# Performance work log

Measured on AMD Instinct MI355X. Metric: run time of the kernel, lower is better.

Reference implementation:

```python
import jax, jax.numpy as jnp
from jax import lax
import numpy as np

CH = 512      # ch_in = c_in = c_out
P = 8         # p: channels per group
NG = CH // P  # depthwise groups
PG = CH // P  # pointwise groups
EPS = 1e-5
DN = ('NCHW', 'OIHW', 'NCHW')


def leaky(x):
    return jnp.where(x >= 0, x, 0.01 * x)  # LeakyReLU default slope


def setup_inputs() -> dict:
    key = jax.random.key(0)
    ks = jax.random.split(key, 8)
    N, H, W = 16, 64, 64
    return {
        'style_encoding': jax.random.normal(ks[0], (N, 512, 4, 4), jnp.float32),
        'content_in': jax.random.normal(ks[1], (N, CH, H, W), jnp.float32),
        'dw_w': jax.random.normal(ks[2], (P, 512, 2, 2), jnp.float32) * 0.05,
        'dw_b': jax.random.normal(ks[3], (P,), jnp.float32) * 0.05,
        'pk_w': jax.random.normal(ks[4], (P, 512), jnp.float32) * 0.05,
        'pk_b': jax.random.normal(ks[5], (P,), jnp.float32) * 0.05,
        'pb_w': jax.random.normal(ks[6], (CH, 512), jnp.float32) * 0.05,
        'pb_b': jax.random.normal(ks[7], (CH,), jnp.float32) * 0.05,
    }


def reference(style_encoding, content_in, dw_w, dw_b, pk_w, pk_b, pb_w, pb_b):
    N, _, H, W = content_in.shape
    # --- KernelPredictor ---
    # depthwise kernels: 2x2 valid conv on 4x4 style map -> [N, P, 3, 3]
    d = lax.conv_general_dilated(style_encoding, dw_w, (1, 1), 'VALID',
                                 dimension_numbers=DN)
    d = leaky(d + dw_b[None, :, None, None])  # [N, P, 3, 3]
    # expand: same [P,3,3] filter for every output channel -> [N, CH, P, 3, 3]
    depthwise = jnp.broadcast_to(d[:, None], (N, CH, P, 3, 3))
    # avg-pool 4 on 4x4 style map == global mean -> [N, 512]
    s_d = jnp.mean(style_encoding, axis=(2, 3))
    pk = jnp.einsum('nc,oc->no', s_d, pk_w) + pk_b       # [N, P]  (1x1 conv)
    bias = jnp.einsum('nc,oc->no', s_d, pb_w) + pb_b     # [N, CH] (1x1 conv)

    # --- per-sample grouped convs, batched by folding batch into groups ---
    padded = jnp.pad(content_in, ((0, 0), (0, 0), (1, 1), (1, 1)), mode='reflect')
    xr = padded.reshape(1, N * CH, H + 2, W + 2)
    wr = depthwise.reshape(N * CH, P, 3, 3)
    depth = lax.conv_general_dilated(xr, wr, (1, 1), 'VALID',
                                     feature_group_count=N * NG,
                                     dimension_numbers=DN)
    depth = depth.reshape(N, CH, H, W)

    # pointwise 1x1 grouped conv: weight [N, CH, P, 1, 1], identical over out
    # channels within a sample (expand); groups = PG, CH//PG == P out ch/group
    depth_g = depth.reshape(N, PG, P, H, W)
    pw_g = jnp.broadcast_to(pk[:, None, None, :], (N, PG, P, P))  # [n,g,o,j]
    out = jnp.einsum('ngjhw,ngoj->ngohw', depth_g, pw_g).reshape(N, CH, H, W)
    predicted = leaky(out + bias[:, :, None, None])

    # --- instance-norm of content (AdaIN calc_mean_std, unbiased var) ---
    mean = jnp.mean(content_in, axis=(2, 3), keepdims=True)
    std = jnp.sqrt(jnp.var(content_in, axis=(2, 3), keepdims=True, ddof=1) + EPS)
    normalized = (content_in - mean) / std
    return normalized * predicted
```

## Files before the change

kernel.cpp:

```cpp
#include <hip/hip_runtime.h>
#include <math.h>

#define CH 512
#define P 8
#define PLANE 4096
#define EPS 1e-5f

typedef float f4 __attribute__((ext_vector_type(4)));

__device__ __forceinline__ float leaky(float x) { return x >= 0.f ? x : 0.01f * x; }

__device__ __forceinline__ float wave_sum(float v) {
    #pragma unroll
    for (int off = 32; off; off >>= 1) v += __shfl_xor(v, off, 64);
    return v;
}

__global__ __launch_bounds__(256) void style_kernel(
    const float* __restrict__ style,
    const float* __restrict__ dw_w,
    const float* __restrict__ dw_b,
    const float* __restrict__ pk_w,
    const float* __restrict__ pk_b,
    float* __restrict__ sd_out,
    float* __restrict__ S_out,
    float* __restrict__ d_pred)
{
    const int blk = blockIdx.x;
    const int t = threadIdx.x;
    const int wave = t >> 6, lane = t & 63;

    __shared__ float s_sd[512];
    __shared__ float red[4];

    if (blk < 16) {
        const int n = blk;
        const float* sb = style + (size_t)n * 8192;
        #pragma unroll
        for (int qd = 0; qd < 2; ++qd) {
            int c = t + 256 * qd;
            const float4* sp = (const float4*)sb + c * 4;
            float4 a = sp[0], b = sp[1], d = sp[2], e = sp[3];
            float s = a.x + a.y + a.z + a.w + b.x + b.y + b.z + b.w
                    + d.x + d.y + d.z + d.w + e.x + e.y + e.z + e.w;
            s *= (1.f / 16.f);
            s_sd[c] = s;
            sd_out[n * 512 + c] = s;
        }
        __syncthreads();
        float part = 0.f;
        #pragma unroll
        for (int o = 0; o < 8; ++o)
            part += pk_w[o * 512 + t] * s_sd[t]
                  + pk_w[o * 512 + t + 256] * s_sd[t + 256];
        part = wave_sum(part);
        if (lane == 0) red[wave] = part;
        __syncthreads();
        if (t == 0) {
            float S = red[0] + red[1] + red[2] + red[3];
            #pragma unroll
            for (int o = 0; o < 8; ++o) S += pk_b[o];
            S_out[n] = S;
        }
    } else {
        const int W = (blk - 16) * 4 + wave;
        const int n = W / 72, r = W % 72;
        const int j = r / 9, pos = r % 9, y = pos / 3, x = pos % 3;
        const float* sb = style + (size_t)n * 8192;
        const float4* wp = (const float4*)dw_w;
        float acc = 0.f;
        #pragma unroll
        for (int i = 0; i < 8; ++i) {
            int c = lane + 64 * i;
            float4 w = wp[j * 512 + c];
            const float* s = sb + c * 16 + y * 4 + x;
            acc += s[0] * w.x + s[1] * w.y + s[4] * w.z + s[5] * w.w;
        }
        acc = wave_sum(acc);
        if (lane == 0) d_pred[n * 72 + r] = leaky(acc + dw_b[j]);
    }
}

__global__ __launch_bounds__(256) void bias_stats_kernel(
    const float* __restrict__ content,
    const float* __restrict__ sd,
    const float* __restrict__ pb_w,
    const float* __restrict__ pb_b,
    float* __restrict__ bias_out,
    float* __restrict__ mean_out,
    float* __restrict__ rstd_out)
{
    const int blk = blockIdx.x;
    const int t = threadIdx.x;
    const int wave = t >> 6, lane = t & 63;

    __shared__ float ls[4], lq[4];

    if (blk < 128) {
        const int c = blk * 4 + wave;
        float w[8];
        #pragma unroll
        for (int i = 0; i < 8; ++i) w[i] = pb_w[(size_t)c * 512 + lane + 64 * i];
        float acc[16];
        #pragma unroll
        for (int nn = 0; nn < 16; ++nn) acc[nn] = 0.f;
        #pragma unroll
        for (int i = 0; i < 8; ++i) {
            #pragma unroll
            for (int nn = 0; nn < 16; ++nn)
                acc[nn] += w[i] * sd[nn * 512 + lane + 64 * i];
        }
        #pragma unroll
        for (int nn = 0; nn < 16; ++nn) acc[nn] = wave_sum(acc[nn]);
        if (lane == 0) {
            float bb = pb_b[c];
            #pragma unroll
            for (int nn = 0; nn < 16; ++nn) bias_out[nn * 512 + c] = acc[nn] + bb;
        }
    } else {
        const int nc = blk - 128;
        const float4* base = (const float4*)(content + (size_t)nc * PLANE);
        float s = 0.f, sq = 0.f;
        #pragma unroll
        for (int k = 0; k < 4; ++k) {
            float4 v = base[k * 256 + t];
            s  += v.x + v.y + v.z + v.w;
            sq += v.x * v.x + v.y * v.y + v.z * v.z + v.w * v.w;
        }
        #pragma unroll
        for (int off = 32; off > 0; off >>= 1) {
            s  += __shfl_down(s, off, 64);
            sq += __shfl_down(sq, off, 64);
        }
        if (lane == 0) { ls[wave] = s; lq[wave] = sq; }
        __syncthreads();
        if (t == 0) {
            float S = ls[0] + ls[1] + ls[2] + ls[3];
            float Q = lq[0] + lq[1] + lq[2] + lq[3];
            float m = S * (1.f / 4096.f);
            float var = (Q - 4096.f * m * m) * (1.f / 4095.f);
            mean_out[nc] = m;
            rstd_out[nc] = rsqrtf(var + EPS);
        }
    }
}

__global__ __launch_bounds__(256, 4) void main_kernel(
    const float* __restrict__ content,
    const float* __restrict__ d_pred,
    const float* __restrict__ S_in,
    const float* __restrict__ bias_in,
    const float* __restrict__ mean_in,
    const float* __restrict__ rstd_in,
    float* __restrict__ out)
{
    const int b    = blockIdx.x;
    const int tile = b & 3;
    const int g    = (b >> 2) & 63;
    const int n    = b >> 8;
    const int t  = threadIdx.x;
    const int tx = t & 15, ty = t >> 4;
    const int h  = tile * 16 + ty;
    const int x0 = tx * 4;

    __shared__ float s_d[72];
    __shared__ float s_S;
    __shared__ float s_bias[8], s_mean[8], s_rstd[8];
    if (t < 72) s_d[t] = d_pred[n * 72 + t];
    if (t == 80) s_S = S_in[n];
    if (t >= 88 && t < 96) {
        int o = t - 88;
        int c = n * 512 + g * 8 + o;
        s_bias[o] = bias_in[c];
        s_mean[o] = mean_in[c];
        s_rstd[o] = rstd_in[c];
    }
    __syncthreads();

    const float* cbase = content + (size_t)(n * 512 + g * 8) * PLANE;
    const int ry0 = (h == 0)  ? 1  : h - 1;
    const int ry2 = (h == 63) ? 62 : h + 1;
    const int o0 = ry0 * 64 + x0;
    const int o1 = h   * 64 + x0;
    const int o2 = ry2 * 64 + x0;

    float D0 = 0.f, D1 = 0.f, D2 = 0.f, D3 = 0.f;
    f4 xc[8];

    #pragma unroll 2
    for (int j = 0; j < 8; ++j) {
        const float* cj = cbase + j * PLANE;
        f4 va = *(const f4*)(cj + o0);
        f4 vb = *(const f4*)(cj + o1);
        f4 vc = *(const f4*)(cj + o2);
        xc[j] = vb;
        const float* wj = s_d + j * 9;
        {
            float lv = __shfl_up(va.w, 1, 64);
            float rv = __shfl_down(va.x, 1, 64);
            float xm = (tx == 0)  ? va.y : lv;
            float xp = (tx == 15) ? va.z : rv;
            D0 += wj[0] * xm   + wj[1] * va.x + wj[2] * va.y;
            D1 += wj[0] * va.x + wj[1] * va.y + wj[2] * va.z;
            D2 += wj[0] * va.y + wj[1] * va.z + wj[2] * va.w;
            D3 += wj[0] * va.z + wj[1] * va.w + wj[2] * xp;
        }
        {
            float lv = __shfl_up(vb.w, 1, 64);
            float rv = __shfl_down(vb.x, 1, 64);
            float xm = (tx == 0)  ? vb.y : lv;
            float xp = (tx == 15) ? vb.z : rv;
            D0 += wj[3] * xm   + wj[4] * vb.x + wj[5] * vb.y;
            D1 += wj[3] * vb.x + wj[4] * vb.y + wj[5] * vb.z;
            D2 += wj[3] * vb.y + wj[4] * vb.z + wj[5] * vb.w;
            D3 += wj[3] * vb.z + wj[4] * vb.w + wj[5] * xp;
        }
        {
            float lv = __shfl_up(vc.w, 1, 64);
            float rv = __shfl_down(vc.x, 1, 64);
            float xm = (tx == 0)  ? vc.y : lv;
            float xp = (tx == 15) ? vc.z : rv;
            D0 += wj[6] * xm   + wj[7] * vc.x + wj[8] * vc.y;
            D1 += wj[6] * vc.x + wj[7] * vc.y + wj[8] * vc.z;
            D2 += wj[6] * vc.y + wj[7] * vc.z + wj[8] * vc.w;
            D3 += wj[6] * vc.z + wj[7] * vc.w + wj[8] * xp;
        }
    }

    const float S = s_S;
    const float P0 = D0 * S, P1 = D1 * S, P2 = D2 * S, P3 = D3 * S;
    float* obase = out + (size_t)(n * 512 + g * 8) * PLANE + h * 64 + x0;
    #pragma unroll
    for (int o = 0; o < 8; ++o) {
        float bb = s_bias[o], m = s_mean[o], rs = s_rstd[o];
        f4 res;
        res.x = (xc[o].x - m) * rs * leaky(P0 + bb);
        res.y = (xc[o].y - m) * rs * leaky(P1 + bb);
        res.z = (xc[o].z - m) * rs * leaky(P2 + bb);
        res.w = (xc[o].w - m) * rs * leaky(P3 + bb);
        __builtin_nontemporal_store(res, (f4*)(obase + o * PLANE));
    }
}

extern "C" void kernel_launch(void* const* d_in, const int* in_sizes, int n_in,
                              void* d_out, int out_size, void* d_ws, size_t ws_size,
                              hipStream_t stream) {
    const float* style   = (const float*)d_in[0];
    const float* content = (const float*)d_in[1];
    const float* dw_w    = (const float*)d_in[2];
    const float* dw_b    = (const float*)d_in[3];
    const float* pk_w    = (const float*)d_in[4];
    const float* pk_b    = (const float*)d_in[5];
    const float* pb_w    = (const float*)d_in[6];
    const float* pb_b    = (const float*)d_in[7];
    float* out = (float*)d_out;
    float* ws  = (float*)d_ws;

    const int N = 16;
    float* sd_ws   = ws;
    float* d_pred  = sd_ws + N * 512;
    float* S_ws    = d_pred + N * 72;
    float* bias_ws = S_ws + N;
    float* mean_ws = bias_ws + N * 512;
    float* rstd_ws = mean_ws + N * 512;

    style_kernel<<<16 + 288, 256, 0, stream>>>(style, dw_w, dw_b, pk_w, pk_b,
                                               sd_ws, S_ws, d_pred);
    bias_stats_kernel<<<128 + N * 512, 256, 0, stream>>>(
        content, sd_ws, pb_w, pb_b, bias_ws, mean_ws, rstd_ws);
    main_kernel<<<N * 64 * 4, 256, 0, stream>>>(content, d_pred, S_ws, bias_ws,
                                                mean_ws, rstd_ws, out);
}
```

Baseline: 265.9 us.

## Merge style and stats kernels; compute bias per block inside main kernel

Folds the content instance-norm statistics into the style prep kernel, which removes one launch and one serialization point. The pointwise-bias GEMV no longer runs as a separate pass: each main-kernel block now computes its own 8 bias values from pb_w and the style means before its barrier. This removes a kernel boundary and the bias workspace round trip. The cost is redundant bias computation, since the four tile blocks of each group and sample each repeat the 8x512 dot products, and that adds latency at block start.

Measured after the change: 266.0 us. About the same (+0.0%).

```diff
diff --git a/kernel.cpp b/kernel.cpp
--- a/kernel.cpp
+++ b/kernel.cpp
@@ -16,15 +16,18 @@
     return v;
 }
 
-__global__ __launch_bounds__(256) void style_kernel(
+__global__ __launch_bounds__(256) void prep_kernel(
     const float* __restrict__ style,
+    const float* __restrict__ content,
     const float* __restrict__ dw_w,
     const float* __restrict__ dw_b,
     const float* __restrict__ pk_w,
     const float* __restrict__ pk_b,
     float* __restrict__ sd_out,
     float* __restrict__ S_out,
-    float* __restrict__ d_pred)
+    float* __restrict__ d_pred,
+    float* __restrict__ mean_out,
+    float* __restrict__ rstd_out)
 {
     const int blk = blockIdx.x;
     const int t = threadIdx.x;
@@ -32,6 +35,7 @@
 
     __shared__ float s_sd[512];
     __shared__ float red[4];
+    __shared__ float ls[4], lq[4];
 
     if (blk < 16) {
         const int n = blk;
@@ -62,7 +66,7 @@
             for (int o = 0; o < 8; ++o) S += pk_b[o];
             S_out[n] = S;
         }
-    } else {
+    } else if (blk < 304) {
         const int W = (blk - 16) * 4 + wave;
         const int n = W / 72, r = W % 72;
         const int j = r / 9, pos = r % 9, y = pos / 3, x = pos % 3;
@@ -78,47 +82,8 @@
         }
         acc = wave_sum(acc);
         if (lane == 0) d_pred[n * 72 + r] = leaky(acc + dw_b[j]);
-    }
-}
-
-__global__ __launch_bounds__(256) void bias_stats_kernel(
-    const float* __restrict__ content,
-    const float* __restrict__ sd,
-    const float* __restrict__ pb_w,
-    const float* __restrict__ pb_b,
-    float* __restrict__ bias_out,
-    float* __restrict__ mean_out,
-    float* __restrict__ rstd_out)
-{
-    const int blk = blockIdx.x;
-    const int t = threadIdx.x;
-    const int wave = t >> 6, lane = t & 63;
-
-    __shared__ float ls[4], lq[4];
-
-    if (blk < 128) {
-        const int c = blk * 4 + wave;
-        float w[8];
-        #pragma unroll
-        for (int i = 0; i < 8; ++i) w[i] = pb_w[(size_t)c * 512 + lane + 64 * i];
-        float acc[16];
-        #pragma unroll
-        for (int nn = 0; nn < 16; ++nn) acc[nn] = 0.f;
-        #pragma unroll
-        for (int i = 0; i < 8; ++i) {
-            #pragma unroll
-            for (int nn = 0; nn < 16; ++nn)
-                acc[nn] += w[i] * sd[nn * 512 + lane + 64 * i];
-        }
-        #pragma unroll
-        for (int nn = 0; nn < 16; ++nn) acc[nn] = wave_sum(acc[nn]);
-        if (lane == 0) {
-            float bb = pb_b[c];
-            #pragma unroll
-            for (int nn = 0; nn < 16; ++nn) bias_out[nn * 512 + c] = acc[nn] + bb;
-        }
     } else {
-        const int nc = blk - 128;
+        const int nc = blk - 304;
         const float4* base = (const float4*)(content + (size_t)nc * PLANE);
         float s = 0.f, sq = 0.f;
         #pragma unroll
@@ -149,7 +114,9 @@
     const float* __restrict__ content,
     const float* __restrict__ d_pred,
     const float* __restrict__ S_in,
-    const float* __restrict__ bias_in,
+    const float* __restrict__ sd,
+    const float* __restrict__ pb_w,
+    const float* __restrict__ pb_b,
     const float* __restrict__ mean_in,
     const float* __restrict__ rstd_in,
     float* __restrict__ out)
@@ -171,9 +138,19 @@
     if (t >= 88 && t < 96) {
         int o = t - 88;
         int c = n * 512 + g * 8 + o;
-        s_bias[o] = bias_in[c];
         s_mean[o] = mean_in[c];
         s_rstd[o] = rstd_in[c];
+    }
+    {
+        const int o = t >> 5, l = t & 31;
+        const float* pw  = pb_w + (size_t)(g * 8 + o) * 512;
+        const float* sdn = sd + n * 512;
+        float acc = 0.f;
+        #pragma unroll
+        for (int i = 0; i < 16; ++i) acc += pw[l + 32 * i] * sdn[l + 32 * i];
+        #pragma unroll
+        for (int off = 16; off; off >>= 1) acc += __shfl_xor(acc, off, 64);
+        if (l == 0) s_bias[o] = acc + pb_b[g * 8 + o];
     }
     __syncthreads();
 
@@ -260,14 +237,12 @@
     float* sd_ws   = ws;
     float* d_pred  = sd_ws + N * 512;
     float* S_ws    = d_pred + N * 72;
-    float* bias_ws = S_ws + N;
-    float* mean_ws = bias_ws + N * 512;
+    float* mean_ws = S_ws + N;
     float* rstd_ws = mean_ws + N * 512;
 
-    style_kernel<<<16 + 288, 256, 0, stream>>>(style, dw_w, dw_b, pk_w, pk_b,
-                                               sd_ws, S_ws, d_pred);
-    bias_stats_kernel<<<128 + N * 512, 256, 0, stream>>>(
-        content, sd_ws, pb_w, pb_b, bias_ws, mean_ws, rstd_ws);
-    main_kernel<<<N * 64 * 4, 256, 0, stream>>>(content, d_pred, S_ws, bias_ws,
-                                                mean_ws, rstd_ws, out);
-}
+    prep_kernel<<<16 + 288 + N * 512, 256, 0, stream>>>(
+        style, content, dw_w, dw_b, pk_w, pk_b,
+        sd_ws, S_ws, d_pred, mean_ws, rstd_ws);
+    main_kernel<<<N * 64 * 4, 256, 0, stream>>>(content, d_pred, S_ws, sd_ws,
+                                                pb_w, pb_b, mean_ws, rstd_ws, out);
+}
```
